# Kernel tuning notes

Measured on AMD Instinct MI355X. Metric: run time of the kernel, lower is better.

Reference implementation:

```python
import jax, jax.numpy as jnp
import numpy as np

GAMMA = 2.0
EPS = 1e-6

B, C = 4096, 32000


def setup_inputs() -> dict:
    key = jax.random.key(0)
    k1, k2 = jax.random.split(key)
    pred = jax.random.normal(k1, (B, C), dtype=jnp.float32)
    target = jax.random.randint(k2, (B,), 0, C, dtype=jnp.int64)
    return {"pred": pred, "target": target}


def reference(pred, target):
    # pred: [B, C] logits, target: [B] int class labels
    b, c = pred.shape
    beta = (b - 1) / b
    logp = jax.nn.log_softmax(pred, axis=1)                      # [B, C]
    # Faithful to original: entropy_b = target_b * sum_c (1-p)^gamma * logp
    # (the torch code multiplies by the scalar class index b_target)
    focal = jnp.sum(jnp.power(1.0 - jnp.exp(logp), GAMMA) * logp, axis=1)  # [B]
    ent = target.astype(pred.dtype) * focal                     # [B]
    # class-balanced aggregation: bucket per class label
    counts = jax.ops.segment_sum(jnp.ones((b,), pred.dtype), target, num_segments=c)  # n_c
    cls_sum = jax.ops.segment_sum(ent, target, num_segments=c)  # sum of entropies per class
    w = (1.0 - beta) / (1.0 - jnp.power(jnp.asarray(beta, pred.dtype), counts) + EPS)
    # classes absent from batch have cls_sum == 0 exactly, so they contribute 0
    return (-1.0 / b) * jnp.sum(w * cls_sum)
```

## Files before the change

kernel.cpp:

```cpp
#include <hip/hip_runtime.h>
#include <math.h>

#define NROWS 4096
#define NCLS  32000
#define VEC_PER_ROW (NCLS / 4)
#define BLK 512
#define NV  16
#define TAIL (VEC_PER_ROW - (NV - 1) * BLK)
#define EPSF 1e-6f
#define LN2  0.69314718055994530942f
#define L2E  1.44269504088896340736f

#define LNBETA (-2.4417042724800387e-4f)
#define WNUM 2.44140625e-4f

#define ROWS_PER_FBLK 16

__device__ __forceinline__ float max4(float4 v) {
    return fmaxf(fmaxf(v.x, v.y), fmaxf(v.z, v.w));
}
__device__ __forceinline__ float sum4(float4 v) {
    return (v.x + v.y) + (v.z + v.w);
}

__global__ __launch_bounds__(BLK, 4) void focal_kernel(const float* __restrict__ pred,
                                                       float* __restrict__ focal_out,
                                                       float* __restrict__ out)
{
    const int row = blockIdx.x;
    const int tid = threadIdx.x;
    if (row == 0 && tid == 0) out[0] = 0.0f;
    const float4* rp = reinterpret_cast<const float4*>(pred) + (size_t)row * VEC_PER_ROW;

    float4 x[NV];
#pragma unroll
    for (int i = 0; i < NV - 1; ++i) x[i] = rp[tid + i * BLK];
    const bool lv = tid < TAIL;
    if (lv) x[NV - 1] = rp[tid + (NV - 1) * BLK];
    else    x[NV - 1] = make_float4(-1e30f, -1e30f, -1e30f, -1e30f);

    float m = -1e30f, s1 = 0.0f;
#pragma unroll
    for (int i = 0; i < NV - 1; ++i) { m = fmaxf(m, max4(x[i])); s1 += sum4(x[i]); }
    m = fmaxf(m, max4(x[NV - 1]));
    if (lv) s1 += sum4(x[NV - 1]);

    __shared__ float sm[8], ss[8];
#pragma unroll
    for (int off = 32; off > 0; off >>= 1) {
        m  = fmaxf(m, __shfl_xor(m, off));
        s1 += __shfl_xor(s1, off);
    }
    const int wid  = tid >> 6;
    const int lane = tid & 63;
    if (lane == 0) { sm[wid] = m; ss[wid] = s1; }
    __syncthreads();
    if (tid < 64) {
        float mm = (tid < 8) ? sm[tid] : -1e30f;
        float s  = (tid < 8) ? ss[tid] : 0.0f;
#pragma unroll
        for (int off = 4; off > 0; off >>= 1) {
            mm = fmaxf(mm, __shfl_xor(mm, off));
            s += __shfl_xor(s, off);
        }
        if (tid == 0) { sm[0] = mm; ss[0] = s; }
    }
    __syncthreads();
    const float M  = sm[0];
    const float S1 = ss[0];

    float Z = 0.f, A = 0.f, Z2 = 0.f, A2 = 0.f;
#pragma unroll
    for (int i = 0; i < NV; ++i) {
        float vals[4] = {x[i].x, x[i].y, x[i].z, x[i].w};
#pragma unroll
        for (int j = 0; j < 4; ++j) {
            float t = vals[j] - M;
            float e = exp2f(t * L2E);
            Z += e;
            A = fmaf(e, t, A);
            float e2 = e * e;
            Z2 += e2;
            A2 = fmaf(e2, t, A2);
        }
    }

    __shared__ float r0[8], r1[8], r2[8], r3[8];
#pragma unroll
    for (int off = 32; off > 0; off >>= 1) {
        Z  += __shfl_xor(Z,  off);
        A  += __shfl_xor(A,  off);
        Z2 += __shfl_xor(Z2, off);
        A2 += __shfl_xor(A2, off);
    }
    if (lane == 0) { r0[wid] = Z; r1[wid] = A; r2[wid] = Z2; r3[wid] = A2; }
    __syncthreads();
    if (tid < 64) {
        float a = (tid < 8) ? r0[tid] : 0.f;
        float b = (tid < 8) ? r1[tid] : 0.f;
        float c = (tid < 8) ? r2[tid] : 0.f;
        float d = (tid < 8) ? r3[tid] : 0.f;
#pragma unroll
        for (int off = 4; off > 0; off >>= 1) {
            a += __shfl_xor(a, off);
            b += __shfl_xor(b, off);
            c += __shfl_xor(c, off);
            d += __shfl_xor(d, off);
        }
        if (tid == 0) {
            float lnZ  = log2f(a) * LN2;
            float invZ = 1.0f / a;
            float T = S1 - (float)NCLS * M;
            float focal = (T - (float)NCLS * lnZ)
                        - 2.0f * (b * invZ - lnZ)
                        + (d - lnZ * c) * (invZ * invZ);
            focal_out[row] = focal;
        }
    }
}

__global__ __launch_bounds__(1024) void finalize_kernel(const int* __restrict__ target,
                                                        const float* __restrict__ focal,
                                                        float* __restrict__ out)
{
    const int tid  = threadIdx.x;
    const int wid  = tid >> 6;
    const int lane = tid & 63;
    const int row  = blockIdx.x * ROWS_PER_FBLK + wid;

    const int t_row = target[row];
    const int4* tg = reinterpret_cast<const int4*>(target);
    int cnt = 0;
#pragma unroll
    for (int k = 0; k < NROWS / 4 / 64; ++k) {
        int4 v = tg[lane + k * 64];
        cnt += (v.x == t_row) + (v.y == t_row) + (v.z == t_row) + (v.w == t_row);
    }
#pragma unroll
    for (int off = 32; off > 0; off >>= 1) cnt += __shfl_xor(cnt, off);

    __shared__ float part[ROWS_PER_FBLK];
    if (lane == 0) {
        float u = (float)cnt * LNBETA;
        float denom;
        if (u > -0.25f) {
            denom = -(u * (1.f + u * (0.5f + u * (0.16666667f + u * 0.041666667f))));
        } else {
            denom = 1.f - __expf(u);
        }
        float w = WNUM / (denom + EPSF);
        part[wid] = w * (float)t_row * focal[row] * (-1.0f / (float)NROWS);
    }
    __syncthreads();
    if (tid == 0) {
        float s = 0.f;
#pragma unroll
        for (int i = 0; i < ROWS_PER_FBLK; ++i) s += part[i];
        atomicAdd(out, s);
    }
}

extern "C" void kernel_launch(void* const* d_in, const int* in_sizes, int n_in,
                              void* d_out, int out_size, void* d_ws, size_t ws_size,
                              hipStream_t stream)
{
    const float* pred  = (const float*)d_in[0];
    const int* target  = (const int*)d_in[1];
    float* out         = (float*)d_out;

    float* focal = (float*)d_ws;

    focal_kernel<<<NROWS, BLK, 0, stream>>>(pred, focal, out);
    finalize_kernel<<<NROWS / ROWS_PER_FBLK, 1024, 0, stream>>>(target, focal, out);
}
```

Before: 101.6 us.

## Make focal kernel persistent with double-buffered register row prefetch

Replaces the one-block-per-row launch of 4096 blocks with 256 persistent blocks of 1024 threads. Each block walks 16 rows strided by the grid size and alternates two register buffers, so the next row's load is issued while the current row is reduced. This is meant to hide memory latency and cut block launch and tail overhead on a purely bandwidth-bound pass. In exchange it doubles the register footprint per thread, and the retained launch bound of four blocks per CU at 1024 threads may push the compiler into tight register limits or spills. Block-wide reductions now cover 16 waves, and an extra barrier is added after each row.

New measurement: 137.2 us. +35.0%, slower.

```diff
diff --git a/kernel.cpp b/kernel.cpp
--- a/kernel.cpp
+++ b/kernel.cpp
@@ -4,9 +4,11 @@
 #define NROWS 4096
 #define NCLS  32000
 #define VEC_PER_ROW (NCLS / 4)
-#define BLK 512
-#define NV  16
-#define TAIL (VEC_PER_ROW - (NV - 1) * BLK)
+#define BLK 1024
+#define NV  8
+#define TAILT (VEC_PER_ROW - (NV - 1) * BLK)
+#define NBLOCKS 256
+#define ROWS_PER_BLK (NROWS / NBLOCKS)
 #define EPSF 1e-6f
 #define LN2  0.69314718055994530942f
 #define L2E  1.44269504088896340736f
@@ -23,43 +25,40 @@
     return (v.x + v.y) + (v.z + v.w);
 }
 
-__global__ __launch_bounds__(BLK, 4) void focal_kernel(const float* __restrict__ pred,
-                                                       float* __restrict__ focal_out,
-                                                       float* __restrict__ out)
-{
-    const int row = blockIdx.x;
-    const int tid = threadIdx.x;
-    if (row == 0 && tid == 0) out[0] = 0.0f;
-    const float4* rp = reinterpret_cast<const float4*>(pred) + (size_t)row * VEC_PER_ROW;
-
-    float4 x[NV];
-#pragma unroll
-    for (int i = 0; i < NV - 1; ++i) x[i] = rp[tid + i * BLK];
-    const bool lv = tid < TAIL;
+__device__ __forceinline__ void load_row(const float4* __restrict__ pred4, int row,
+                                         int tid, bool lv, float4 (&x)[NV])
+{
+    const float4* rp = pred4 + (size_t)row * VEC_PER_ROW;
+#pragma unroll
+    for (int k = 0; k < NV - 1; ++k) x[k] = rp[tid + k * BLK];
     if (lv) x[NV - 1] = rp[tid + (NV - 1) * BLK];
     else    x[NV - 1] = make_float4(-1e30f, -1e30f, -1e30f, -1e30f);
-
+}
+
+__device__ __forceinline__ void compute_row(const float4 (&x)[NV], bool lv, int row,
+                                            int tid, int wid, int lane,
+                                            float* sm, float* ss,
+                                            float* r0, float* r1, float* r2, float* r3,
+                                            float* __restrict__ focal_out)
+{
     float m = -1e30f, s1 = 0.0f;
 #pragma unroll
     for (int i = 0; i < NV - 1; ++i) { m = fmaxf(m, max4(x[i])); s1 += sum4(x[i]); }
     m = fmaxf(m, max4(x[NV - 1]));
     if (lv) s1 += sum4(x[NV - 1]);
 
-    __shared__ float sm[8], ss[8];
 #pragma unroll
     for (int off = 32; off > 0; off >>= 1) {
         m  = fmaxf(m, __shfl_xor(m, off));
         s1 += __shfl_xor(s1, off);
     }
-    const int wid  = tid >> 6;
-    const int lane = tid & 63;
     if (lane == 0) { sm[wid] = m; ss[wid] = s1; }
     __syncthreads();
     if (tid < 64) {
-        float mm = (tid < 8) ? sm[tid] : -1e30f;
-        float s  = (tid < 8) ? ss[tid] : 0.0f;
-#pragma unroll
-        for (int off = 4; off > 0; off >>= 1) {
+        float mm = (tid < 16) ? sm[tid] : -1e30f;
+        float s  = (tid < 16) ? ss[tid] : 0.0f;
+#pragma unroll
+        for (int off = 8; off > 0; off >>= 1) {
             mm = fmaxf(mm, __shfl_xor(mm, off));
             s += __shfl_xor(s, off);
         }
@@ -85,7 +84,6 @@
         }
     }
 
-    __shared__ float r0[8], r1[8], r2[8], r3[8];
 #pragma unroll
     for (int off = 32; off > 0; off >>= 1) {
         Z  += __shfl_xor(Z,  off);
@@ -96,12 +94,12 @@
     if (lane == 0) { r0[wid] = Z; r1[wid] = A; r2[wid] = Z2; r3[wid] = A2; }
     __syncthreads();
     if (tid < 64) {
-        float a = (tid < 8) ? r0[tid] : 0.f;
-        float b = (tid < 8) ? r1[tid] : 0.f;
-        float c = (tid < 8) ? r2[tid] : 0.f;
-        float d = (tid < 8) ? r3[tid] : 0.f;
-#pragma unroll
-        for (int off = 4; off > 0; off >>= 1) {
+        float a = (tid < 16) ? r0[tid] : 0.f;
+        float b = (tid < 16) ? r1[tid] : 0.f;
+        float c = (tid < 16) ? r2[tid] : 0.f;
+        float d = (tid < 16) ? r3[tid] : 0.f;
+#pragma unroll
+        for (int off = 8; off > 0; off >>= 1) {
             a += __shfl_xor(a, off);
             b += __shfl_xor(b, off);
             c += __shfl_xor(c, off);
@@ -117,6 +115,36 @@
             focal_out[row] = focal;
         }
     }
+    __syncthreads();
+}
+
+__global__ __launch_bounds__(BLK, 4) void focal_kernel(const float* __restrict__ pred,
+                                                       float* __restrict__ focal_out,
+                                                       float* __restrict__ out)
+{
+    const int bid  = blockIdx.x;
+    const int tid  = threadIdx.x;
+    const int wid  = tid >> 6;
+    const int lane = tid & 63;
+    const bool lv  = tid < TAILT;
+    if (bid == 0 && tid == 0) out[0] = 0.0f;
+
+    __shared__ float sm[16], ss[16], r0[16], r1[16], r2[16], r3[16];
+
+    const float4* pred4 = reinterpret_cast<const float4*>(pred);
+
+    float4 xa[NV], xb[NV];
+    load_row(pred4, bid, tid, lv, xa);
+
+    for (int i = 0; i < ROWS_PER_BLK; i += 2) {
+        const int rowA = bid + NBLOCKS * i;
+        const int rowB = bid + NBLOCKS * (i + 1);
+        load_row(pred4, rowB, tid, lv, xb);
+        compute_row(xa, lv, rowA, tid, wid, lane, sm, ss, r0, r1, r2, r3, focal_out);
+        if (i + 2 < ROWS_PER_BLK)
+            load_row(pred4, bid + NBLOCKS * (i + 2), tid, lv, xa);
+        compute_row(xb, lv, rowB, tid, wid, lane, sm, ss, r0, r1, r2, r3, focal_out);
+    }
 }
 
 __global__ __launch_bounds__(1024) void finalize_kernel(const int* __restrict__ target,
@@ -170,6 +198,6 @@
 
     float* focal = (float*)d_ws;
 
-    focal_kernel<<<NROWS, BLK, 0, stream>>>(pred, focal, out);
+    focal_kernel<<<NBLOCKS, BLK, 0, stream>>>(pred, focal, out);
     finalize_kernel<<<NROWS / ROWS_PER_FBLK, 1024, 0, stream>>>(target, focal, out);
 }
```
